# Kernel tuning notes

Measured on AMD Instinct MI355X. Metric: run time of the kernel, lower is better.

The kernel has to match this reference:

```python
import jax, jax.numpy as jnp
import numpy as np

N_NODES = 50000
N_HEDGES = 100000
N_INC = 600000
F_IN = 512
HID = 128
EPS = 1e-5
ALPHA = 0.5


def layer_norm(x, g, b):
    mu = jnp.mean(x, axis=-1, keepdims=True)
    var = jnp.mean((x - mu) ** 2, axis=-1, keepdims=True)
    return (x - mu) * jax.lax.rsqrt(var + EPS) * g + b


def scatter_mean(src, idx, num_segments):
    s = jax.ops.segment_sum(src, idx, num_segments=num_segments)
    c = jax.ops.segment_sum(jnp.ones((src.shape[0], 1), src.dtype), idx, num_segments=num_segments)
    return jnp.where(c > 0, s / jnp.maximum(c, 1.0), 0.0)


def setup_inputs() -> dict:
    key = jax.random.key(0)
    ks = jax.random.split(key, 20)

    def lin(k, fi, fo):
        kw, kb = jax.random.split(k)
        w = jax.random.normal(kw, (fi, fo), jnp.float32) / np.sqrt(fi)
        b = jax.random.normal(kb, (fo,), jnp.float32) * 0.01
        return w, b

    x1 = jax.random.normal(ks[0], (N_NODES, F_IN), jnp.float32)
    x2 = jax.random.normal(ks[1], (N_NODES, F_IN), jnp.float32)
    v1 = jax.random.randint(ks[2], (N_INC,), 0, N_NODES, jnp.int32)
    e1 = jax.random.randint(ks[3], (N_INC,), 0, N_HEDGES, jnp.int32)
    v2 = jax.random.randint(ks[4], (N_INC,), 0, N_NODES, jnp.int32)
    e2 = jax.random.randint(ks[5], (N_INC,), 0, N_HEDGES, jnp.int32)

    lin_w, lin_b = lin(ks[6], F_IN, HID)
    w1_w, w1_b = lin(ks[7], HID, HID)
    w2_w, w2_b = lin(ks[8], 2 * HID, HID)
    w_w, w_b = lin(ks[9], HID, HID)
    cls_w1, cls_b1 = lin(ks[10], HID, 64)
    cls_w2, cls_b2 = lin(ks[11], 64, 1)

    return {
        "x1": x1, "v1": v1, "e1": e1, "x2": x2, "v2": v2, "e2": e2,
        "lin_w": lin_w, "lin_b": lin_b,
        "w1_ln_g": jnp.ones((HID,)), "w1_ln_b": jnp.zeros((HID,)), "w1_w": w1_w, "w1_b": w1_b,
        "w2_ln_g": jnp.ones((2 * HID,)), "w2_ln_b": jnp.zeros((2 * HID,)), "w2_w": w2_w, "w2_b": w2_b,
        "w_ln_g": jnp.ones((HID,)), "w_ln_b": jnp.zeros((HID,)), "w_w": w_w, "w_b": w_b,
        "cls_w1": cls_w1, "cls_b1": cls_b1,
        "cls_ln_g": jnp.ones((64,)), "cls_ln_b": jnp.zeros((64,)),
        "cls_w2": cls_w2, "cls_b2": cls_b2,
    }


def _conv(X, v, e, X0, p):
    # W1 (LN + Linear) on vertices, gather to incidence pairs
    Xve = (layer_norm(X, p["w1_ln_g"], p["w1_ln_b"]) @ p["w1_w"] + p["w1_b"])[v]  # [E, H]
    Xe = scatter_mean(Xve, e, N_HEDGES)                                             # [M, H]
    Xev = Xe[e]                                                                      # [E, H]
    cat = jnp.concatenate([X[v], Xev], axis=-1)                                      # [E, 2H]
    Xev = layer_norm(cat, p["w2_ln_g"], p["w2_ln_b"]) @ p["w2_w"] + p["w2_b"]      # [E, H]
    Xv = scatter_mean(Xev, v, X.shape[0])                                            # [N, H]
    X = (1.0 - ALPHA) * Xv + ALPHA * X0
    return layer_norm(X, p["w_ln_g"], p["w_ln_b"]) @ p["w_w"] + p["w_b"]


def _branch(x, v, e, p):
    x = jax.nn.relu(x @ p["lin_w"] + p["lin_b"])
    x0 = x
    for _ in range(2):  # nlayer=2, shared conv weights
        x = jax.nn.relu(_conv(x, v, e, x0, p))
    # classifier MLP: Linear -> relu -> LN -> Linear
    h = jax.nn.relu(x @ p["cls_w1"] + p["cls_b1"])
    h = layer_norm(h, p["cls_ln_g"], p["cls_ln_b"])
    return h @ p["cls_w2"] + p["cls_b2"]


def reference(x1, v1, e1, x2, v2, e2,
              lin_w, lin_b,
              w1_ln_g, w1_ln_b, w1_w, w1_b,
              w2_ln_g, w2_ln_b, w2_w, w2_b,
              w_ln_g, w_ln_b, w_w, w_b,
              cls_w1, cls_b1, cls_ln_g, cls_ln_b, cls_w2, cls_b2):
    p = dict(lin_w=lin_w, lin_b=lin_b,
             w1_ln_g=w1_ln_g, w1_ln_b=w1_ln_b, w1_w=w1_w, w1_b=w1_b,
             w2_ln_g=w2_ln_g, w2_ln_b=w2_ln_b, w2_w=w2_w, w2_b=w2_b,
             w_ln_g=w_ln_g, w_ln_b=w_ln_b, w_w=w_w, w_b=w_b,
             cls_w1=cls_w1, cls_b1=cls_b1, cls_ln_g=cls_ln_g, cls_ln_b=cls_ln_b,
             cls_w2=cls_w2, cls_b2=cls_b2)
    return (_branch(x1, v1, e1, p), _branch(x2, v2, e2, p))
```

## Files before the change

### kernel.cpp

```cpp
#include <hip/hip_runtime.h>

#define NN 50000
#define NH 100000
#define NI 600000
#define FIN 512
#define HID 128
#define LNEPS 1e-5f

static __device__ __forceinline__ void fma4(float4& a, float s, const float4& w) {
  a.x += s * w.x; a.y += s * w.y; a.z += s * w.z; a.w += s * w.w;
}
static __device__ __forceinline__ float f4c(const float4& a, int k) {
  return k == 0 ? a.x : k == 1 ? a.y : k == 2 ? a.z : a.w;
}

__global__ void k_hist(const int* __restrict__ idx, int n, int* __restrict__ deg) {
  int i = blockIdx.x * 256 + threadIdx.x;
  if (i < n) atomicAdd(&deg[idx[i]], 1);
}

__global__ __launch_bounds__(1024) void k_scan1(int* __restrict__ data, int m,
                                                int* __restrict__ bsums) {
  __shared__ int sh[1024];
  int tid = threadIdx.x;
  int i = blockIdx.x * 1024 + tid;
  int v = (i < m) ? data[i] : 0;
  sh[tid] = v;
  __syncthreads();
  for (int off = 1; off < 1024; off <<= 1) {
    int tv = (tid >= off) ? sh[tid - off] : 0;
    __syncthreads();
    sh[tid] += tv;
    __syncthreads();
  }
  if (i < m) data[i] = sh[tid] - v;
  if (tid == 1023) bsums[blockIdx.x] = sh[1023];
}

__global__ __launch_bounds__(1024) void k_scan2(int* __restrict__ bsums, int nb) {
  __shared__ int sh[1024];
  int tid = threadIdx.x;
  int v = (tid < nb) ? bsums[tid] : 0;
  sh[tid] = v;
  __syncthreads();
  for (int off = 1; off < 1024; off <<= 1) {
    int tv = (tid >= off) ? sh[tid - off] : 0;
    __syncthreads();
    sh[tid] += tv;
    __syncthreads();
  }
  if (tid < nb) bsums[tid] = sh[tid] - v;
}

__global__ void k_scan3(int* __restrict__ data, const int* __restrict__ bsums,
                        int m, int total) {
  int i = blockIdx.x * 256 + threadIdx.x;
  if (i < m) data[i] += bsums[i >> 10];
  if (i == 0) data[m] = total;
}

__global__ void k_fill(const int* __restrict__ key, const int* __restrict__ oth, int n,
                       const int* __restrict__ starts, int* __restrict__ cursor,
                       int* __restrict__ out_oth) {
  int i = blockIdx.x * 256 + threadIdx.x;
  if (i >= n) return;
  int k = key[i];
  int pos = starts[k] + atomicAdd(&cursor[k], 1);
  out_oth[pos] = oth[i];
}

__global__ void k_sort_seg(const int* __restrict__ starts, int nseg,
                           int* __restrict__ vals) {
  int seg = blockIdx.x * 256 + threadIdx.x;
  if (seg >= nseg) return;
  int s = starts[seg], e = starts[seg + 1];
  int d = e - s;
  if (d <= 1) return;
  if (d <= 48) {
    int buf[48];
    for (int i = 0; i < d; i++) buf[i] = vals[s + i];
    for (int i = 1; i < d; i++) {
      int key = buf[i], j = i - 1;
      while (j >= 0 && buf[j] > key) { buf[j + 1] = buf[j]; j--; }
      buf[j + 1] = key;
    }
    for (int i = 0; i < d; i++) vals[s + i] = buf[i];
  } else {
    for (int i = s + 1; i < e; i++) {
      int key = vals[i], j = i - 1;
      while (j >= s && vals[j] > key) { vals[j + 1] = vals[j]; j--; }
      vals[j + 1] = key;
    }
  }
}

__global__ void k_prep_w2g(const float* __restrict__ W2, const float* __restrict__ g2,
                           float* __restrict__ W2g) {
  int i = blockIdx.x * 256 + threadIdx.x;
  if (i >= 256 * 128) return;
  int k = i >> 7;
  W2g[i] = g2[k] * W2[i];
}

__global__ __launch_bounds__(128) void k_prep_sgc0(
    const float* __restrict__ W2, const float* __restrict__ g2,
    const float* __restrict__ b2, const float* __restrict__ bias2,
    float* __restrict__ s_g, float* __restrict__ c0) {
  int t = threadIdx.x;
  float sg = 0.f, cc = 0.f;
  for (int k = 0; k < 256; k++) {
    float w = W2[k * 128 + t];
    sg += g2[k] * w;
    cc += b2[k] * w;
  }
  s_g[t] = sg;
  c0[t] = cc + bias2[t];
}

static __device__ __forceinline__ void stage_w16(float (*Wsh)[132], const float* __restrict__ W,
                                                 int row0, int t) {
  for (int s = t; s < 512; s += 256) {
    int k = s >> 5, c4 = (s & 31) * 4;
    *(float4*)&Wsh[k][c4] = *(const float4*)(W + (size_t)(row0 + k) * 128 + c4);
  }
}

static __device__ __forceinline__ void gemm128(const float (*Ash)[132], float (*Wsh)[132],
                                               const float* __restrict__ W,
                                               int t, int tc, int tr,
                                               float4 acc0[2], float4 acc1[2]) {
  for (int kk = 0; kk < 8; kk++) {
    __syncthreads();
    stage_w16(Wsh, W, kk * 16, t);
    __syncthreads();
    const int kb = kk * 16;
#pragma unroll
    for (int k4 = 0; k4 < 16; k4 += 4) {
      float4 a0 = *(const float4*)&Ash[tr * 2 + 0][kb + k4];
      float4 a1 = *(const float4*)&Ash[tr * 2 + 1][kb + k4];
#pragma unroll
      for (int kk2 = 0; kk2 < 4; kk2++) {
        float4 w0 = *(const float4*)&Wsh[k4 + kk2][tc * 4];
        float4 w1 = *(const float4*)&Wsh[k4 + kk2][64 + tc * 4];
        float a0v = f4c(a0, kk2), a1v = f4c(a1, kk2);
        fma4(acc0[0], a0v, w0); fma4(acc0[1], a0v, w1);
        fma4(acc1[0], a1v, w0); fma4(acc1[1], a1v, w1);
      }
    }
  }
}

static __device__ __forceinline__ void stage_w(float (*Wsh)[68], const float* __restrict__ W,
                                               int ldw, int row0, int col0, int t) {
  for (int s = t; s < 512; s += 256) {
    int k = s >> 4, c4 = (s & 15) * 4;
    *(float4*)&Wsh[k][c4] = *(const float4*)(W + (size_t)(row0 + k) * ldw + col0 + c4);
  }
}

static __device__ __forceinline__ void inner32(const float (*Ash)[132], const float (*Wsh)[68],
                                               int kb, int tc, int tr,
                                               float4& acc0, float4& acc1) {
#pragma unroll
  for (int k = 0; k < 32; k += 4) {
    float4 w0 = *(const float4*)&Wsh[k + 0][tc * 4];
    float4 w1 = *(const float4*)&Wsh[k + 1][tc * 4];
    float4 w2 = *(const float4*)&Wsh[k + 2][tc * 4];
    float4 w3 = *(const float4*)&Wsh[k + 3][tc * 4];
    float4 a0 = *(const float4*)&Ash[tr * 2 + 0][kb + k];
    float4 a1 = *(const float4*)&Ash[tr * 2 + 1][kb + k];
    fma4(acc0, a0.x, w0); fma4(acc0, a0.y, w1); fma4(acc0, a0.z, w2); fma4(acc0, a0.w, w3);
    fma4(acc1, a1.x, w0); fma4(acc1, a1.y, w1); fma4(acc1, a1.z, w2); fma4(acc1, a1.w, w3);
  }
}

static __device__ __forceinline__ void load_a128(float (*Ash)[132], const float* __restrict__ A,
                                                 int r0, int N, int t) {
  for (int s = t; s < 1024; s += 256) {
    int r = s >> 5, c4 = (s & 31) * 4;
    float4 val = {0, 0, 0, 0};
    if (r0 + r < N) val = *(const float4*)(A + (size_t)(r0 + r) * 128 + c4);
    *(float4*)&Ash[r][c4] = val;
  }
}

template <bool STATS>
static __device__ __forceinline__ void ln_tile(float (*Ash)[132], const float* __restrict__ g,
                                               const float* __restrict__ b,
                                               float* __restrict__ sn, float* __restrict__ qn,
                                               int r0, int N, int t) {
  int wv = t >> 6, lane = t & 63;
  for (int j = 0; j < 8; j++) {
    int r = wv * 8 + j;
    if (r0 + r < N) {
      float2 x = *(float2*)&Ash[r][lane * 2];
      float s = x.x + x.y, sq = x.x * x.x + x.y * x.y;
      for (int m = 1; m < 64; m <<= 1) { s += __shfl_xor(s, m); sq += __shfl_xor(sq, m); }
      if (STATS && lane == 0) { sn[r0 + r] = s; qn[r0 + r] = sq; }
      float mu = s * (1.f / 128.f);
      float var = sq * (1.f / 128.f) - mu * mu;
      float rstd = rsqrtf(var + LNEPS);
      float2 gg = ((const float2*)g)[lane];
      float2 bb = ((const float2*)b)[lane];
      float2 o;
      o.x = (x.x - mu) * rstd * gg.x + bb.x;
      o.y = (x.y - mu) * rstd * gg.y + bb.y;
      *(float2*)&Ash[r][lane * 2] = o;
    }
  }
}

__global__ __launch_bounds__(256) void k_proj_fused(
    const float* __restrict__ x_in, const float* __restrict__ lin_w,
    const float* __restrict__ lin_b, const float* __restrict__ w1g,
    const float* __restrict__ w1bn, const float* __restrict__ w1w,
    const float* __restrict__ w1b, float* __restrict__ X0,
    float* __restrict__ B, float* __restrict__ sn, float* __restrict__ qn, int N) {
  __shared__ float Ash[32][132];
  __shared__ float Wsh[32][68];
  float (*W16)[132] = (float(*)[132])Wsh;
  const int t = threadIdx.x;
  const int r0 = blockIdx.x * 32;
  const int tc = t & 15, tr = t >> 4;
  float4 acc0[2] = {{0,0,0,0},{0,0,0,0}}, acc1[2] = {{0,0,0,0},{0,0,0,0}};
  for (int kq = 0; kq < 4; kq++) {
    __syncthreads();
    for (int s = t; s < 1024; s += 256) {
      int r = s >> 5, c4 = (s & 31) * 4;
      float4 val = {0, 0, 0, 0};
      if (r0 + r < N) val = *(const float4*)(x_in + (size_t)(r0 + r) * 512 + kq * 128 + c4);
      *(float4*)&Ash[r][c4] = val;
    }
    gemm128((const float(*)[132])Ash, W16, lin_w + (size_t)kq * 128 * 128, t, tc, tr,
            acc0, acc1);
  }
  __syncthreads();
  for (int h = 0; h < 2; h++) {
    int c = h * 64 + tc * 4;
    float4 bb = *(const float4*)(lin_b + c);
    int row0 = r0 + tr * 2;
    float4 z0, z1;
    z0.x = fmaxf(acc0[h].x + bb.x, 0.f); z0.y = fmaxf(acc0[h].y + bb.y, 0.f);
    z0.z = fmaxf(acc0[h].z + bb.z, 0.f); z0.w = fmaxf(acc0[h].w + bb.w, 0.f);
    z1.x = fmaxf(acc1[h].x + bb.x, 0.f); z1.y = fmaxf(acc1[h].y + bb.y, 0.f);
    z1.z = fmaxf(acc1[h].z + bb.z, 0.f); z1.w = fmaxf(acc1[h].w + bb.w, 0.f);
    if (row0 < N) {
      *(float4*)(X0 + (size_t)row0 * 128 + c) = z0;
      *(float4*)&Ash[tr * 2][c] = z0;
    }
    if (row0 + 1 < N) {
      *(float4*)(X0 + (size_t)(row0 + 1) * 128 + c) = z1;
      *(float4*)&Ash[tr * 2 + 1][c] = z1;
    }
  }
  __syncthreads();
  ln_tile<true>(Ash, w1g, w1bn, sn, qn, r0, N, t);
  float4 f0[2] = {{0,0,0,0},{0,0,0,0}}, f1[2] = {{0,0,0,0},{0,0,0,0}};
  gemm128((const float(*)[132])Ash, W16, w1w, t, tc, tr, f0, f1);
  for (int h = 0; h < 2; h++) {
    int c = h * 64 + tc * 4;
    float4 bb = *(const float4*)(w1b + c);
    int row0 = r0 + tr * 2;
    if (row0 < N) {
      float4 o = {f0[h].x + bb.x, f0[h].y + bb.y, f0[h].z + bb.z, f0[h].w + bb.w};
      *(float4*)(B + (size_t)row0 * 128 + c) = o;
    }
    if (row0 + 1 < N) {
      float4 o = {f1[h].x + bb.x, f1[h].y + bb.y, f1[h].z + bb.z, f1[h].w + bb.w};
      *(float4*)(B + (size_t)(row0 + 1) * 128 + c) = o;
    }
  }
}

__global__ __launch_bounds__(256) void k_xe(
    const float* __restrict__ B, const int* __restrict__ starts,
    const int* __restrict__ vlist, float* __restrict__ Xe,
    float* __restrict__ se, float* __restrict__ qe, int M) {
  int half = threadIdx.x >> 5, lane = threadIdx.x & 31;
  int m = blockIdx.x * 8 + half;
  if (m >= M) return;
  int s = starts[m], e = starts[m + 1];
  float4 acc = {0.f, 0.f, 0.f, 0.f};
  for (int j = s; j < e; j++) {
    int vv = vlist[j];
    float4 val = ((const float4*)(B + (size_t)vv * 128))[lane];
    acc.x += val.x; acc.y += val.y; acc.z += val.z; acc.w += val.w;
  }
  int d = e - s;
  float inv = d > 0 ? 1.f / (float)d : 0.f;
  float4 o = {acc.x * inv, acc.y * inv, acc.z * inv, acc.w * inv};
  ((float4*)(Xe + (size_t)m * 128))[lane] = o;
  float ss = o.x + o.y + o.z + o.w;
  float qq = o.x * o.x + o.y * o.y + o.z * o.z + o.w * o.w;
  for (int mm = 1; mm < 32; mm <<= 1) {
    ss += __shfl_xor(ss, mm, 32);
    qq += __shfl_xor(qq, mm, 32);
  }
  if (lane == 0) { se[m] = ss; qe[m] = qq; }
}

__global__ __launch_bounds__(256) void k_nodeg(
    const float* __restrict__ X, const float* __restrict__ Xe,
    const int* __restrict__ starts_v, const int* __restrict__ e_by_v,
    const float* __restrict__ sn, const float* __restrict__ qn,
    const float* __restrict__ se, const float* __restrict__ qe,
    float* __restrict__ P, float* __restrict__ Qb,
    float* __restrict__ invdeg, float* __restrict__ t2arr, int N) {
  int half = threadIdx.x >> 5, lane = threadIdx.x & 31;
  int v = blockIdx.x * 8 + half;
  if (v >= N) return;
  int s = starts_v[v], e = starts_v[v + 1];
  float svn = sn[v], qvn = qn[v];
  float4 acc = {0.f, 0.f, 0.f, 0.f};
  float suma = 0.f, sumb = 0.f;
  for (int j = s; j < e; j++) {
    int ee = e_by_v[j];
    float mu = (svn + se[ee]) * (1.f / 256.f);
    float e2 = (qvn + qe[ee]) * (1.f / 256.f);
    float rstd = rsqrtf(e2 - mu * mu + LNEPS);
    suma += rstd;
    sumb += mu * rstd;
    float4 vv = ((const float4*)(Xe + (size_t)ee * 128))[lane];
    acc.x += rstd * vv.x; acc.y += rstd * vv.y;
    acc.z += rstd * vv.z; acc.w += rstd * vv.w;
  }
  float4 xr = ((const float4*)(X + (size_t)v * 128))[lane];
  float4 pp = {suma * xr.x, suma * xr.y, suma * xr.z, suma * xr.w};
  ((float4*)(P + (size_t)v * 128))[lane] = pp;
  ((float4*)(Qb + (size_t)v * 128))[lane] = acc;
  if (lane == 0) {
    int d = e - s;
    float inv = d > 0 ? 1.f / (float)d : 0.f;
    invdeg[v] = inv;
    t2arr[v] = sumb * inv;
  }
}

static __device__ __forceinline__ void conv2_body(
    float (*Ash)[132], float (*Wsh)[132],
    const float* __restrict__ P, const float* __restrict__ Q,
    const float* __restrict__ W, const float* __restrict__ invdeg,
    const float* __restrict__ t2arr, const float* __restrict__ s_g,
    const float* __restrict__ c0, const float* __restrict__ X0,
    const float* __restrict__ wg, const float* __restrict__ wbn,
    int r0, int N, int t, int tc, int tr) {
  float4 acc0[2] = {{0,0,0,0},{0,0,0,0}}, acc1[2] = {{0,0,0,0},{0,0,0,0}};
  for (int ph = 0; ph < 2; ph++) {
    __syncthreads();
    load_a128(Ash, ph ? Q : P, r0, N, t);
    gemm128((const float(*)[132])Ash, Wsh, W + (size_t)ph * 128 * 128, t, tc, tr,
            acc0, acc1);
  }
  __syncthreads();
  for (int r = 0; r < 2; r++) {
    int row = r0 + tr * 2 + r;
    if (row < N) {
      float t1 = invdeg[row], t2 = t2arr[row];
      float flag = t1 > 0.f ? 1.f : 0.f;
      for (int h = 0; h < 2; h++) {
        int c = h * 64 + tc * 4;
        float4 g = r ? acc1[h] : acc0[h];
        float4 sg = *(const float4*)(s_g + c);
        float4 cc = *(const float4*)(c0 + c);
        float4 x0 = *(const float4*)(X0 + (size_t)row * 128 + c);
        float4 z;
        z.x = 0.5f * (g.x * t1 - t2 * sg.x + flag * cc.x) + 0.5f * x0.x;
        z.y = 0.5f * (g.y * t1 - t2 * sg.y + flag * cc.y) + 0.5f * x0.y;
        z.z = 0.5f * (g.z * t1 - t2 * sg.z + flag * cc.z) + 0.5f * x0.z;
        z.w = 0.5f * (g.w * t1 - t2 * sg.w + flag * cc.w) + 0.5f * x0.w;
        *(float4*)&Ash[tr * 2 + r][c] = z;
      }
    }
  }
  __syncthreads();
  ln_tile<false>(Ash, wg, wbn, nullptr, nullptr, r0, N, t);
}

__global__ __launch_bounds__(256) void k_conv2w(
    const float* __restrict__ P, const float* __restrict__ Q,
    const float* __restrict__ W, const float* __restrict__ invdeg,
    const float* __restrict__ t2arr, const float* __restrict__ s_g,
    const float* __restrict__ c0, const float* __restrict__ X0,
    const float* __restrict__ wg, const float* __restrict__ wbn,
    const float* __restrict__ Ww, const float* __restrict__ wb,
    const float* __restrict__ w1g, const float* __restrict__ w1bn,
    const float* __restrict__ w1w, const float* __restrict__ w1b,
    float* __restrict__ Xout, float* __restrict__ B,
    float* __restrict__ sn, float* __restrict__ qn, int N) {
  __shared__ float Ash[32][132];
  __shared__ float Wsh[32][68];
  float (*W16)[132] = (float(*)[132])Wsh;
  const int t = threadIdx.x;
  const int r0 = blockIdx.x * 32;
  const int tc = t & 15, tr = t >> 4;
  conv2_body(Ash, W16, P, Q, W, invdeg, t2arr, s_g, c0, X0, wg, wbn, r0, N, t, tc, tr);
  float4 b0[2] = {{0,0,0,0},{0,0,0,0}}, b1[2] = {{0,0,0,0},{0,0,0,0}};
  gemm128((const float(*)[132])Ash, W16, Ww, t, tc, tr, b0, b1);
  __syncthreads();
  for (int h = 0; h < 2; h++) {
    int c = h * 64 + tc * 4;
    float4 bb = *(const float4*)(wb + c);
    int row0 = r0 + tr * 2;
    float4 z0, z1;
    z0.x = fmaxf(b0[h].x + bb.x, 0.f); z0.y = fmaxf(b0[h].y + bb.y, 0.f);
    z0.z = fmaxf(b0[h].z + bb.z, 0.f); z0.w = fmaxf(b0[h].w + bb.w, 0.f);
    z1.x = fmaxf(b1[h].x + bb.x, 0.f); z1.y = fmaxf(b1[h].y + bb.y, 0.f);
    z1.z = fmaxf(b1[h].z + bb.z, 0.f); z1.w = fmaxf(b1[h].w + bb.w, 0.f);
    if (row0 < N) {
      *(float4*)(Xout + (size_t)row0 * 128 + c) = z0;
      *(float4*)&Ash[tr * 2][c] = z0;
    }
    if (row0 + 1 < N) {
      *(float4*)(Xout + (size_t)(row0 + 1) * 128 + c) = z1;
      *(float4*)&Ash[tr * 2 + 1][c] = z1;
    }
  }
  __syncthreads();
  ln_tile<true>(Ash, w1g, w1bn, sn, qn, r0, N, t);
  float4 f0[2] = {{0,0,0,0},{0,0,0,0}}, f1[2] = {{0,0,0,0},{0,0,0,0}};
  gemm128((const float(*)[132])Ash, W16, w1w, t, tc, tr, f0, f1);
  for (int h = 0; h < 2; h++) {
    int c = h * 64 + tc * 4;
    float4 bb = *(const float4*)(w1b + c);
    int row0 = r0 + tr * 2;
    if (row0 < N) {
      float4 o = {f0[h].x + bb.x, f0[h].y + bb.y, f0[h].z + bb.z, f0[h].w + bb.w};
      *(float4*)(B + (size_t)row0 * 128 + c) = o;
    }
    if (row0 + 1 < N) {
      float4 o = {f1[h].x + bb.x, f1[h].y + bb.y, f1[h].z + bb.z, f1[h].w + bb.w};
      *(float4*)(B + (size_t)(row0 + 1) * 128 + c) = o;
    }
  }
}

__global__ __launch_bounds__(256) void k_conv2c(
    const float* __restrict__ P, const float* __restrict__ Q,
    const float* __restrict__ W, const float* __restrict__ invdeg,
    const float* __restrict__ t2arr, const float* __restrict__ s_g,
    const float* __restrict__ c0, const float* __restrict__ X0,
    const float* __restrict__ wg, const float* __restrict__ wbn,
    const float* __restrict__ Ww, const float* __restrict__ wb,
    const float* __restrict__ cw1, const float* __restrict__ cb1,
    const float* __restrict__ cg, const float* __restrict__ cbn,
    const float* __restrict__ cw2, const float* __restrict__ cb2,
    float* __restrict__ out, int N) {
  __shared__ float Ash[32][132];
  __shared__ float Wsh[32][68];
  float (*W16)[132] = (float(*)[132])Wsh;
  const int t = threadIdx.x;
  const int r0 = blockIdx.x * 32;
  const int tc = t & 15, tr = t >> 4;
  conv2_body(Ash, W16, P, Q, W, invdeg, t2arr, s_g, c0, X0, wg, wbn, r0, N, t, tc, tr);
  float4 b0[2] = {{0,0,0,0},{0,0,0,0}}, b1[2] = {{0,0,0,0},{0,0,0,0}};
  gemm128((const float(*)[132])Ash, W16, Ww, t, tc, tr, b0, b1);
  __syncthreads();
  for (int h = 0; h < 2; h++) {
    int c = h * 64 + tc * 4;
    float4 bb = *(const float4*)(wb + c);
    int row0 = r0 + tr * 2;
    if (row0 < N) {
      float4 z;
      z.x = fmaxf(b0[h].x + bb.x, 0.f); z.y = fmaxf(b0[h].y + bb.y, 0.f);
      z.z = fmaxf(b0[h].z + bb.z, 0.f); z.w = fmaxf(b0[h].w + bb.w, 0.f);
      *(float4*)&Ash[tr * 2][c] = z;
    }
    if (row0 + 1 < N) {
      float4 z;
      z.x = fmaxf(b1[h].x + bb.x, 0.f); z.y = fmaxf(b1[h].y + bb.y, 0.f);
      z.z = fmaxf(b1[h].z + bb.z, 0.f); z.w = fmaxf(b1[h].w + bb.w, 0.f);
      *(float4*)&Ash[tr * 2 + 1][c] = z;
    }
  }
  float4 h0 = {0,0,0,0}, h1 = {0,0,0,0};
  for (int kc = 0; kc < 4; kc++) {
    __syncthreads();
    stage_w(Wsh, cw1, 64, kc * 32, 0, t);
    __syncthreads();
    inner32((const float(*)[132])Ash, (const float(*)[68])Wsh, kc * 32, tc, tr, h0, h1);
  }
  __syncthreads();
  {
    int c = tc * 4;
    float4 bb = *(const float4*)(cb1 + c);
    float4 z;
    z.x = fmaxf(h0.x + bb.x, 0.f); z.y = fmaxf(h0.y + bb.y, 0.f);
    z.z = fmaxf(h0.z + bb.z, 0.f); z.w = fmaxf(h0.w + bb.w, 0.f);
    *(float4*)&Wsh[tr * 2][c] = z;
    z.x = fmaxf(h1.x + bb.x, 0.f); z.y = fmaxf(h1.y + bb.y, 0.f);
    z.z = fmaxf(h1.z + bb.z, 0.f); z.w = fmaxf(h1.w + bb.w, 0.f);
    *(float4*)&Wsh[tr * 2 + 1][c] = z;
  }
  __syncthreads();
  int wv = t >> 6, lane = t & 63;
  for (int j = 0; j < 8; j++) {
    int r = wv * 8 + j;
    if (r0 + r < N) {
      float h = Wsh[r][lane];
      float s = h, sq = h * h;
      for (int m = 1; m < 64; m <<= 1) { s += __shfl_xor(s, m); sq += __shfl_xor(sq, m); }
      float mu = s * (1.f / 64.f);
      float var = sq * (1.f / 64.f) - mu * mu;
      float rstd = rsqrtf(var + LNEPS);
      float hn = (h - mu) * rstd * cg[lane] + cbn[lane];
      float c = hn * cw2[lane];
      for (int m = 1; m < 64; m <<= 1) c += __shfl_xor(c, m);
      if (lane == 0) out[r0 + r] = c + cb2[0];
    }
  }
}

static void run_branch(const float* x_in, const int* v, const int* e,
                       const float* lin_w, const float* lin_b,
                       const float* w1g, const float* w1bn, const float* w1w, const float* w1b,
                       const float* W2g, const float* s_g, const float* c0,
                       const float* wg, const float* wbn, const float* ww, const float* wb,
                       const float* cw1, const float* cb1, const float* cg, const float* cbn,
                       const float* cw2, const float* cb2,
                       float* X, float* X0, float* B, float* Qb, float* Xe,
                       float* sn, float* qn, float* se, float* qe,
                       float* invdeg, float* t2arr,
                       int* starts_e, int* starts_v, int* cursor, int* bsums,
                       int* v_by_e, int* e_by_v,
                       float* out, hipStream_t stream) {
  const int GN = (NN + 31) / 32;
  hipMemsetAsync(starts_e, 0, (NH + 1) * sizeof(int), stream);
  k_hist<<<(NI + 255) / 256, 256, 0, stream>>>(e, NI, starts_e);
  k_scan1<<<(NH + 1023) / 1024, 1024, 0, stream>>>(starts_e, NH, bsums);
  k_scan2<<<1, 1024, 0, stream>>>(bsums, (NH + 1023) / 1024);
  k_scan3<<<(NH + 255) / 256, 256, 0, stream>>>(starts_e, bsums, NH, NI);
  hipMemsetAsync(cursor, 0, NH * sizeof(int), stream);
  k_fill<<<(NI + 255) / 256, 256, 0, stream>>>(e, v, NI, starts_e, cursor, v_by_e);
  k_sort_seg<<<(NH + 255) / 256, 256, 0, stream>>>(starts_e, NH, v_by_e);
  hipMemsetAsync(starts_v, 0, (NN + 1) * sizeof(int), stream);
  k_hist<<<(NI + 255) / 256, 256, 0, stream>>>(v, NI, starts_v);
  k_scan1<<<(NN + 1023) / 1024, 1024, 0, stream>>>(starts_v, NN, bsums);
  k_scan2<<<1, 1024, 0, stream>>>(bsums, (NN + 1023) / 1024);
  k_scan3<<<(NN + 255) / 256, 256, 0, stream>>>(starts_v, bsums, NN, NI);
  hipMemsetAsync(cursor, 0, NN * sizeof(int), stream);
  k_fill<<<(NI + 255) / 256, 256, 0, stream>>>(v, e, NI, starts_v, cursor, e_by_v);
  k_sort_seg<<<(NN + 255) / 256, 256, 0, stream>>>(starts_v, NN, e_by_v);
  k_proj_fused<<<GN, 256, 0, stream>>>(x_in, lin_w, lin_b, w1g, w1bn, w1w, w1b,
                                       X0, B, sn, qn, NN);
  for (int layer = 0; layer < 2; ++layer) {
    k_xe<<<NH / 8, 256, 0, stream>>>(B, starts_e, v_by_e, Xe, se, qe, NH);
    k_nodeg<<<(NN + 7) / 8, 256, 0, stream>>>(layer == 0 ? X0 : X, Xe, starts_v,
                                              e_by_v, sn, qn, se, qe, B, Qb,
                                              invdeg, t2arr, NN);
    if (layer == 0) {
      k_conv2w<<<GN, 256, 0, stream>>>(B, Qb, W2g, invdeg, t2arr, s_g, c0, X0,
                                       wg, wbn, ww, wb, w1g, w1bn, w1w, w1b,
                                       X, B, sn, qn, NN);
    } else {
      k_conv2c<<<GN, 256, 0, stream>>>(B, Qb, W2g, invdeg, t2arr, s_g, c0, X0,
                                       wg, wbn, ww, wb, cw1, cb1, cg, cbn,
                                       cw2, cb2, out, NN);
    }
  }
}

extern "C" void kernel_launch(void* const* d_in, const int* in_sizes, int n_in,
                              void* d_out, int out_size, void* d_ws, size_t ws_size,
                              hipStream_t stream) {
  (void)in_sizes; (void)n_in; (void)out_size; (void)ws_size;
  const float* x1 = (const float*)d_in[0];
  const int* v1 = (const int*)d_in[1];
  const int* e1 = (const int*)d_in[2];
  const float* x2 = (const float*)d_in[3];
  const int* v2 = (const int*)d_in[4];
  const int* e2 = (const int*)d_in[5];
  const float* lin_w = (const float*)d_in[6];
  const float* lin_b = (const float*)d_in[7];
  const float* w1g = (const float*)d_in[8];
  const float* w1bn = (const float*)d_in[9];
  const float* w1w = (const float*)d_in[10];
  const float* w1b = (const float*)d_in[11];
  const float* w2g = (const float*)d_in[12];
  const float* w2bn = (const float*)d_in[13];
  const float* w2w = (const float*)d_in[14];
  const float* w2b = (const float*)d_in[15];
  const float* wg = (const float*)d_in[16];
  const float* wbn = (const float*)d_in[17];
  const float* ww = (const float*)d_in[18];
  const float* wb = (const float*)d_in[19];
  const float* cw1 = (const float*)d_in[20];
  const float* cb1 = (const float*)d_in[21];
  const float* cg = (const float*)d_in[22];
  const float* cbn = (const float*)d_in[23];
  const float* cw2 = (const float*)d_in[24];
  const float* cb2 = (const float*)d_in[25];

  char* p = (char*)d_ws;
  auto alloc = [&](size_t bytes) {
    char* r = p;
    p += (bytes + 255) & ~(size_t)255;
    return r;
  };
  float* X = (float*)alloc((size_t)NN * 128 * 4);
  float* X0 = (float*)alloc((size_t)NN * 128 * 4);
  float* B = (float*)alloc((size_t)NN * 128 * 4);
  float* Qb = (float*)alloc((size_t)NN * 128 * 4);
  float* Xe = (float*)alloc((size_t)NH * 128 * 4);
  float* sn = (float*)alloc((size_t)NN * 4);
  float* qn = (float*)alloc((size_t)NN * 4);
  float* se = (float*)alloc((size_t)NH * 4);
  float* qe = (float*)alloc((size_t)NH * 4);
  float* invdeg = (float*)alloc((size_t)NN * 4);
  float* t2arr = (float*)alloc((size_t)NN * 4);
  int* starts_e = (int*)alloc((NH + 1) * 4);
  int* starts_v = (int*)alloc((NN + 1) * 4);
  int* cursor = (int*)alloc(NH * 4);
  int* bsums = (int*)alloc(1024 * 4);
  int* v_by_e = (int*)alloc((size_t)NI * 4);
  int* e_by_v = (int*)alloc((size_t)NI * 4);
  float* W2g = (float*)alloc((size_t)256 * 128 * 4);
  float* s_g = (float*)alloc(128 * 4);
  float* c0 = (float*)alloc(128 * 4);

  k_prep_w2g<<<128, 256, 0, stream>>>(w2w, w2g, W2g);
  k_prep_sgc0<<<1, 128, 0, stream>>>(w2w, w2g, w2bn, w2b, s_g, c0);

  float* out = (float*)d_out;
  run_branch(x1, v1, e1, lin_w, lin_b, w1g, w1bn, w1w, w1b, W2g, s_g, c0,
             wg, wbn, ww, wb, cw1, cb1, cg, cbn, cw2, cb2,
             X, X0, B, Qb, Xe, sn, qn, se, qe, invdeg, t2arr,
             starts_e, starts_v, cursor, bsums, v_by_e, e_by_v, out, stream);
  run_branch(x2, v2, e2, lin_w, lin_b, w1g, w1bn, w1w, w1b, W2g, s_g, c0,
             wg, wbn, ww, wb, cw1, cb1, cg, cbn, cw2, cb2,
             X, X0, B, Qb, Xe, sn, qn, se, qe, invdeg, t2arr,
             starts_e, starts_v, cursor, bsums, v_by_e, e_by_v, out + NN, stream);
}
```

Measured before the change: 1.784 ms.

## Batch CSR construction for both branches and drop P buffer write in nodeg

Builds the incidence CSR structures (histogram, scan, fill, segment sort) for both branches in shared launches, each with a doubled grid, instead of running them sequentially per branch. This halves the number of small preprocessing launches and gives each one more parallel work. Separately, k_nodeg no longer writes the P = suma*X matrix; it stores a per-node suma scalar, and the conv kernel scales X while loading the tile. That removes one full N×128 write and reread, at the cost of a few extra workspace buffers for the second branch's CSR.

```diff
diff --git a/kernel.cpp b/kernel.cpp
--- a/kernel.cpp
+++ b/kernel.cpp
@@ -14,16 +14,27 @@
   return k == 0 ? a.x : k == 1 ? a.y : k == 2 ? a.z : a.w;
 }
 
-__global__ void k_hist(const int* __restrict__ idx, int n, int* __restrict__ deg) {
-  int i = blockIdx.x * 256 + threadIdx.x;
+__global__ void k_hist2(const int* __restrict__ i1, const int* __restrict__ i2, int n,
+                        int* __restrict__ d1, int* __restrict__ d2) {
+  int nb = gridDim.x >> 1, blk = blockIdx.x;
+  bool a = blk < nb;
+  const int* idx = a ? i1 : i2;
+  int* deg = a ? d1 : d2;
+  int i = (a ? blk : blk - nb) * 256 + threadIdx.x;
   if (i < n) atomicAdd(&deg[idx[i]], 1);
 }
 
-__global__ __launch_bounds__(1024) void k_scan1(int* __restrict__ data, int m,
-                                                int* __restrict__ bsums) {
+__global__ __launch_bounds__(1024) void k_scan1_2(int* __restrict__ dd1, int* __restrict__ dd2,
+                                                  int m, int* __restrict__ b1,
+                                                  int* __restrict__ b2) {
   __shared__ int sh[1024];
+  int nb = gridDim.x >> 1, blk = blockIdx.x;
+  bool a = blk < nb;
+  int* data = a ? dd1 : dd2;
+  int* bsums = a ? b1 : b2;
+  int lb = a ? blk : blk - nb;
   int tid = threadIdx.x;
-  int i = blockIdx.x * 1024 + tid;
+  int i = lb * 1024 + tid;
   int v = (i < m) ? data[i] : 0;
   sh[tid] = v;
   __syncthreads();
@@ -34,11 +45,13 @@
     __syncthreads();
   }
   if (i < m) data[i] = sh[tid] - v;
-  if (tid == 1023) bsums[blockIdx.x] = sh[1023];
-}
-
-__global__ __launch_bounds__(1024) void k_scan2(int* __restrict__ bsums, int nb) {
+  if (tid == 1023) bsums[lb] = sh[1023];
+}
+
+__global__ __launch_bounds__(1024) void k_scan2_2(int* __restrict__ b1, int* __restrict__ b2,
+                                                  int nb) {
   __shared__ int sh[1024];
+  int* bsums = blockIdx.x == 0 ? b1 : b2;
   int tid = threadIdx.x;
   int v = (tid < nb) ? bsums[tid] : 0;
   sh[tid] = v;
@@ -52,26 +65,44 @@
   if (tid < nb) bsums[tid] = sh[tid] - v;
 }
 
-__global__ void k_scan3(int* __restrict__ data, const int* __restrict__ bsums,
-                        int m, int total) {
-  int i = blockIdx.x * 256 + threadIdx.x;
-  if (i < m) data[i] += bsums[i >> 10];
+__global__ void k_scan3_2(int* __restrict__ dd1, int* __restrict__ dd2,
+                          const int* __restrict__ b1, const int* __restrict__ b2,
+                          int m, int total) {
+  int nb = gridDim.x >> 1, blk = blockIdx.x;
+  bool a = blk < nb;
+  int* data = a ? dd1 : dd2;
+  const int* bs = a ? b1 : b2;
+  int i = (a ? blk : blk - nb) * 256 + threadIdx.x;
+  if (i < m) data[i] += bs[i >> 10];
   if (i == 0) data[m] = total;
 }
 
-__global__ void k_fill(const int* __restrict__ key, const int* __restrict__ oth, int n,
-                       const int* __restrict__ starts, int* __restrict__ cursor,
-                       int* __restrict__ out_oth) {
-  int i = blockIdx.x * 256 + threadIdx.x;
+__global__ void k_fill2(const int* __restrict__ k1, const int* __restrict__ o1,
+                        const int* __restrict__ k2, const int* __restrict__ o2, int n,
+                        const int* __restrict__ s1, const int* __restrict__ s2,
+                        int* __restrict__ c1, int* __restrict__ c2,
+                        int* __restrict__ out1, int* __restrict__ out2) {
+  int nb = gridDim.x >> 1, blk = blockIdx.x;
+  bool a = blk < nb;
+  const int* key = a ? k1 : k2;
+  const int* oth = a ? o1 : o2;
+  const int* st = a ? s1 : s2;
+  int* cur = a ? c1 : c2;
+  int* out = a ? out1 : out2;
+  int i = (a ? blk : blk - nb) * 256 + threadIdx.x;
   if (i >= n) return;
   int k = key[i];
-  int pos = starts[k] + atomicAdd(&cursor[k], 1);
-  out_oth[pos] = oth[i];
-}
-
-__global__ void k_sort_seg(const int* __restrict__ starts, int nseg,
-                           int* __restrict__ vals) {
-  int seg = blockIdx.x * 256 + threadIdx.x;
+  int pos = st[k] + atomicAdd(&cur[k], 1);
+  out[pos] = oth[i];
+}
+
+__global__ void k_sort2(const int* __restrict__ s1, const int* __restrict__ s2, int nseg,
+                        int* __restrict__ v1, int* __restrict__ v2) {
+  int nb = gridDim.x >> 1, blk = blockIdx.x;
+  bool a = blk < nb;
+  const int* starts = a ? s1 : s2;
+  int* vals = a ? v1 : v2;
+  int seg = (a ? blk : blk - nb) * 256 + threadIdx.x;
   if (seg >= nseg) return;
   int s = starts[seg], e = starts[seg + 1];
   int d = e - s;
@@ -180,6 +211,21 @@
     int r = s >> 5, c4 = (s & 31) * 4;
     float4 val = {0, 0, 0, 0};
     if (r0 + r < N) val = *(const float4*)(A + (size_t)(r0 + r) * 128 + c4);
+    *(float4*)&Ash[r][c4] = val;
+  }
+}
+
+static __device__ __forceinline__ void load_a128s(float (*Ash)[132], const float* __restrict__ A,
+                                                  const float* __restrict__ scale,
+                                                  int r0, int N, int t) {
+  for (int s = t; s < 1024; s += 256) {
+    int r = s >> 5, c4 = (s & 31) * 4;
+    float4 val = {0, 0, 0, 0};
+    if (r0 + r < N) {
+      float sc = scale[r0 + r];
+      float4 x = *(const float4*)(A + (size_t)(r0 + r) * 128 + c4);
+      val.x = sc * x.x; val.y = sc * x.y; val.z = sc * x.z; val.w = sc * x.w;
+    }
     *(float4*)&Ash[r][c4] = val;
   }
 }
@@ -300,12 +346,12 @@
 }
 
 __global__ __launch_bounds__(256) void k_nodeg(
-    const float* __restrict__ X, const float* __restrict__ Xe,
-    const int* __restrict__ starts_v, const int* __restrict__ e_by_v,
-    const float* __restrict__ sn, const float* __restrict__ qn,
-    const float* __restrict__ se, const float* __restrict__ qe,
-    float* __restrict__ P, float* __restrict__ Qb,
-    float* __restrict__ invdeg, float* __restrict__ t2arr, int N) {
+    const float* __restrict__ Xe, const int* __restrict__ starts_v,
+    const int* __restrict__ e_by_v, const float* __restrict__ sn,
+    const float* __restrict__ qn, const float* __restrict__ se,
+    const float* __restrict__ qe, float* __restrict__ Qb,
+    float* __restrict__ suma_arr, float* __restrict__ invdeg,
+    float* __restrict__ t2arr, int N) {
   int half = threadIdx.x >> 5, lane = threadIdx.x & 31;
   int v = blockIdx.x * 8 + half;
   if (v >= N) return;
@@ -324,13 +370,11 @@
     acc.x += rstd * vv.x; acc.y += rstd * vv.y;
     acc.z += rstd * vv.z; acc.w += rstd * vv.w;
   }
-  float4 xr = ((const float4*)(X + (size_t)v * 128))[lane];
-  float4 pp = {suma * xr.x, suma * xr.y, suma * xr.z, suma * xr.w};
-  ((float4*)(P + (size_t)v * 128))[lane] = pp;
   ((float4*)(Qb + (size_t)v * 128))[lane] = acc;
   if (lane == 0) {
     int d = e - s;
     float inv = d > 0 ? 1.f / (float)d : 0.f;
+    suma_arr[v] = suma;
     invdeg[v] = inv;
     t2arr[v] = sumb * inv;
   }
@@ -338,16 +382,17 @@
 
 static __device__ __forceinline__ void conv2_body(
     float (*Ash)[132], float (*Wsh)[132],
-    const float* __restrict__ P, const float* __restrict__ Q,
-    const float* __restrict__ W, const float* __restrict__ invdeg,
-    const float* __restrict__ t2arr, const float* __restrict__ s_g,
-    const float* __restrict__ c0, const float* __restrict__ X0,
-    const float* __restrict__ wg, const float* __restrict__ wbn,
-    int r0, int N, int t, int tc, int tr) {
+    const float* __restrict__ Xsrc, const float* __restrict__ suma,
+    const float* __restrict__ Q, const float* __restrict__ W,
+    const float* __restrict__ invdeg, const float* __restrict__ t2arr,
+    const float* __restrict__ s_g, const float* __restrict__ c0,
+    const float* __restrict__ X0, const float* __restrict__ wg,
+    const float* __restrict__ wbn, int r0, int N, int t, int tc, int tr) {
   float4 acc0[2] = {{0,0,0,0},{0,0,0,0}}, acc1[2] = {{0,0,0,0},{0,0,0,0}};
   for (int ph = 0; ph < 2; ph++) {
     __syncthreads();
-    load_a128(Ash, ph ? Q : P, r0, N, t);
+    if (ph == 0) load_a128s(Ash, Xsrc, suma, r0, N, t);
+    else load_a128(Ash, Q, r0, N, t);
     gemm128((const float(*)[132])Ash, Wsh, W + (size_t)ph * 128 * 128, t, tc, tr,
             acc0, acc1);
   }
@@ -377,23 +422,24 @@
 }
 
 __global__ __launch_bounds__(256) void k_conv2w(
-    const float* __restrict__ P, const float* __restrict__ Q,
-    const float* __restrict__ W, const float* __restrict__ invdeg,
-    const float* __restrict__ t2arr, const float* __restrict__ s_g,
-    const float* __restrict__ c0, const float* __restrict__ X0,
-    const float* __restrict__ wg, const float* __restrict__ wbn,
-    const float* __restrict__ Ww, const float* __restrict__ wb,
-    const float* __restrict__ w1g, const float* __restrict__ w1bn,
-    const float* __restrict__ w1w, const float* __restrict__ w1b,
-    float* __restrict__ Xout, float* __restrict__ B,
-    float* __restrict__ sn, float* __restrict__ qn, int N) {
+    const float* __restrict__ Xsrc, const float* __restrict__ suma,
+    const float* __restrict__ Q, const float* __restrict__ W,
+    const float* __restrict__ invdeg, const float* __restrict__ t2arr,
+    const float* __restrict__ s_g, const float* __restrict__ c0,
+    const float* __restrict__ X0, const float* __restrict__ wg,
+    const float* __restrict__ wbn, const float* __restrict__ Ww,
+    const float* __restrict__ wb, const float* __restrict__ w1g,
+    const float* __restrict__ w1bn, const float* __restrict__ w1w,
+    const float* __restrict__ w1b, float* __restrict__ Xout,
+    float* __restrict__ B, float* __restrict__ sn, float* __restrict__ qn, int N) {
   __shared__ float Ash[32][132];
   __shared__ float Wsh[32][68];
   float (*W16)[132] = (float(*)[132])Wsh;
   const int t = threadIdx.x;
   const int r0 = blockIdx.x * 32;
   const int tc = t & 15, tr = t >> 4;
-  conv2_body(Ash, W16, P, Q, W, invdeg, t2arr, s_g, c0, X0, wg, wbn, r0, N, t, tc, tr);
+  conv2_body(Ash, W16, Xsrc, suma, Q, W, invdeg, t2arr, s_g, c0, X0, wg, wbn,
+             r0, N, t, tc, tr);
   float4 b0[2] = {{0,0,0,0},{0,0,0,0}}, b1[2] = {{0,0,0,0},{0,0,0,0}};
   gemm128((const float(*)[132])Ash, W16, Ww, t, tc, tr, b0, b1);
   __syncthreads();
@@ -435,23 +481,24 @@
 }
 
 __global__ __launch_bounds__(256) void k_conv2c(
-    const float* __restrict__ P, const float* __restrict__ Q,
-    const float* __restrict__ W, const float* __restrict__ invdeg,
-    const float* __restrict__ t2arr, const float* __restrict__ s_g,
-    const float* __restrict__ c0, const float* __restrict__ X0,
-    const float* __restrict__ wg, const float* __restrict__ wbn,
-    const float* __restrict__ Ww, const float* __restrict__ wb,
-    const float* __restrict__ cw1, const float* __restrict__ cb1,
-    const float* __restrict__ cg, const float* __restrict__ cbn,
-    const float* __restrict__ cw2, const float* __restrict__ cb2,
-    float* __restrict__ out, int N) {
+    const float* __restrict__ Xsrc, const float* __restrict__ suma,
+    const float* __restrict__ Q, const float* __restrict__ W,
+    const float* __restrict__ invdeg, const float* __restrict__ t2arr,
+    const float* __restrict__ s_g, const float* __restrict__ c0,
+    const float* __restrict__ X0, const float* __restrict__ wg,
+    const float* __restrict__ wbn, const float* __restrict__ Ww,
+    const float* __restrict__ wb, const float* __restrict__ cw1,
+    const float* __restrict__ cb1, const float* __restrict__ cg,
+    const float* __restrict__ cbn, const float* __restrict__ cw2,
+    const float* __restrict__ cb2, float* __restrict__ out, int N) {
   __shared__ float Ash[32][132];
   __shared__ float Wsh[32][68];
   float (*W16)[132] = (float(*)[132])Wsh;
   const int t = threadIdx.x;
   const int r0 = blockIdx.x * 32;
   const int tc = t & 15, tr = t >> 4;
-  conv2_body(Ash, W16, P, Q, W, invdeg, t2arr, s_g, c0, X0, wg, wbn, r0, N, t, tc, tr);
+  conv2_body(Ash, W16, Xsrc, suma, Q, W, invdeg, t2arr, s_g, c0, X0, wg, wbn,
+             r0, N, t, tc, tr);
   float4 b0[2] = {{0,0,0,0},{0,0,0,0}}, b1[2] = {{0,0,0,0},{0,0,0,0}};
   gemm128((const float(*)[132])Ash, W16, Ww, t, tc, tr, b0, b1);
   __syncthreads();
@@ -510,7 +557,7 @@
   }
 }
 
-static void run_branch(const float* x_in, const int* v, const int* e,
+static void run_branch(const float* x_in,
                        const float* lin_w, const float* lin_b,
                        const float* w1g, const float* w1bn, const float* w1w, const float* w1b,
                        const float* W2g, const float* s_g, const float* c0,
@@ -519,41 +566,25 @@
                        const float* cw2, const float* cb2,
                        float* X, float* X0, float* B, float* Qb, float* Xe,
                        float* sn, float* qn, float* se, float* qe,
-                       float* invdeg, float* t2arr,
-                       int* starts_e, int* starts_v, int* cursor, int* bsums,
-                       int* v_by_e, int* e_by_v,
+                       float* suma, float* invdeg, float* t2arr,
+                       const int* starts_e, const int* starts_v,
+                       const int* v_by_e, const int* e_by_v,
                        float* out, hipStream_t stream) {
   const int GN = (NN + 31) / 32;
-  hipMemsetAsync(starts_e, 0, (NH + 1) * sizeof(int), stream);
-  k_hist<<<(NI + 255) / 256, 256, 0, stream>>>(e, NI, starts_e);
-  k_scan1<<<(NH + 1023) / 1024, 1024, 0, stream>>>(starts_e, NH, bsums);
-  k_scan2<<<1, 1024, 0, stream>>>(bsums, (NH + 1023) / 1024);
-  k_scan3<<<(NH + 255) / 256, 256, 0, stream>>>(starts_e, bsums, NH, NI);
-  hipMemsetAsync(cursor, 0, NH * sizeof(int), stream);
-  k_fill<<<(NI + 255) / 256, 256, 0, stream>>>(e, v, NI, starts_e, cursor, v_by_e);
-  k_sort_seg<<<(NH + 255) / 256, 256, 0, stream>>>(starts_e, NH, v_by_e);
-  hipMemsetAsync(starts_v, 0, (NN + 1) * sizeof(int), stream);
-  k_hist<<<(NI + 255) / 256, 256, 0, stream>>>(v, NI, starts_v);
-  k_scan1<<<(NN + 1023) / 1024, 1024, 0, stream>>>(starts_v, NN, bsums);
-  k_scan2<<<1, 1024, 0, stream>>>(bsums, (NN + 1023) / 1024);
-  k_scan3<<<(NN + 255) / 256, 256, 0, stream>>>(starts_v, bsums, NN, NI);
-  hipMemsetAsync(cursor, 0, NN * sizeof(int), stream);
-  k_fill<<<(NI + 255) / 256, 256, 0, stream>>>(v, e, NI, starts_v, cursor, e_by_v);
-  k_sort_seg<<<(NN + 255) / 256, 256, 0, stream>>>(starts_v, NN, e_by_v);
   k_proj_fused<<<GN, 256, 0, stream>>>(x_in, lin_w, lin_b, w1g, w1bn, w1w, w1b,
                                        X0, B, sn, qn, NN);
   for (int layer = 0; layer < 2; ++layer) {
+    const float* Xsrc = layer == 0 ? X0 : X;
     k_xe<<<NH / 8, 256, 0, stream>>>(B, starts_e, v_by_e, Xe, se, qe, NH);
-    k_nodeg<<<(NN + 7) / 8, 256, 0, stream>>>(layer == 0 ? X0 : X, Xe, starts_v,
-                                              e_by_v, sn, qn, se, qe, B, Qb,
-                                              invdeg, t2arr, NN);
+    k_nodeg<<<(NN + 7) / 8, 256, 0, stream>>>(Xe, starts_v, e_by_v, sn, qn, se, qe,
+                                              Qb, suma, invdeg, t2arr, NN);
     if (layer == 0) {
-      k_conv2w<<<GN, 256, 0, stream>>>(B, Qb, W2g, invdeg, t2arr, s_g, c0, X0,
-                                       wg, wbn, ww, wb, w1g, w1bn, w1w, w1b,
+      k_conv2w<<<GN, 256, 0, stream>>>(Xsrc, suma, Qb, W2g, invdeg, t2arr, s_g, c0,
+                                       X0, wg, wbn, ww, wb, w1g, w1bn, w1w, w1b,
                                        X, B, sn, qn, NN);
     } else {
-      k_conv2c<<<GN, 256, 0, stream>>>(B, Qb, W2g, invdeg, t2arr, s_g, c0, X0,
-                                       wg, wbn, ww, wb, cw1, cb1, cg, cbn,
+      k_conv2c<<<GN, 256, 0, stream>>>(Xsrc, suma, Qb, W2g, invdeg, t2arr, s_g, c0,
+                                       X0, wg, wbn, ww, wb, cw1, cb1, cg, cbn,
                                        cw2, cb2, out, NN);
     }
   }
@@ -605,28 +636,65 @@
   float* qn = (float*)alloc((size_t)NN * 4);
   float* se = (float*)alloc((size_t)NH * 4);
   float* qe = (float*)alloc((size_t)NH * 4);
+  float* suma = (float*)alloc((size_t)NN * 4);
   float* invdeg = (float*)alloc((size_t)NN * 4);
   float* t2arr = (float*)alloc((size_t)NN * 4);
-  int* starts_e = (int*)alloc((NH + 1) * 4);
-  int* starts_v = (int*)alloc((NN + 1) * 4);
-  int* cursor = (int*)alloc(NH * 4);
-  int* bsums = (int*)alloc(1024 * 4);
-  int* v_by_e = (int*)alloc((size_t)NI * 4);
-  int* e_by_v = (int*)alloc((size_t)NI * 4);
+  int* starts_e_all = (int*)alloc((size_t)2 * (NH + 1) * 4);
+  int* starts_v_all = (int*)alloc((size_t)2 * (NN + 1) * 4);
+  int* cursor_all = (int*)alloc((size_t)2 * NH * 4);
+  int* bsums_all = (int*)alloc((size_t)2 * 1024 * 4);
+  int* v_by_e1 = (int*)alloc((size_t)NI * 4);
+  int* v_by_e2 = (int*)alloc((size_t)NI * 4);
+  int* e_by_v1 = (int*)alloc((size_t)NI * 4);
+  int* e_by_v2 = (int*)alloc((size_t)NI * 4);
   float* W2g = (float*)alloc((size_t)256 * 128 * 4);
   float* s_g = (float*)alloc(128 * 4);
   float* c0 = (float*)alloc(128 * 4);
 
+  int* se1 = starts_e_all;
+  int* se2 = starts_e_all + (NH + 1);
+  int* sv1 = starts_v_all;
+  int* sv2 = starts_v_all + (NN + 1);
+  int* cur1 = cursor_all;
+  int* cur2 = cursor_all + NH;
+  int* bs1 = bsums_all;
+  int* bs2 = bsums_all + 1024;
+
   k_prep_w2g<<<128, 256, 0, stream>>>(w2w, w2g, W2g);
   k_prep_sgc0<<<1, 128, 0, stream>>>(w2w, w2g, w2bn, w2b, s_g, c0);
 
+  const int GBI = (NI + 255) / 256;
+  const int GBE = (NH + 1023) / 1024;
+  const int GBV = (NN + 1023) / 1024;
+  const int GHE = (NH + 255) / 256;
+  const int GHV = (NN + 255) / 256;
+
+  hipMemsetAsync(starts_e_all, 0, (size_t)2 * (NH + 1) * 4, stream);
+  k_hist2<<<2 * GBI, 256, 0, stream>>>(e1, e2, NI, se1, se2);
+  k_scan1_2<<<2 * GBE, 1024, 0, stream>>>(se1, se2, NH, bs1, bs2);
+  k_scan2_2<<<2, 1024, 0, stream>>>(bs1, bs2, GBE);
+  k_scan3_2<<<2 * GHE, 256, 0, stream>>>(se1, se2, bs1, bs2, NH, NI);
+  hipMemsetAsync(cursor_all, 0, (size_t)2 * NH * 4, stream);
+  k_fill2<<<2 * GBI, 256, 0, stream>>>(e1, v1, e2, v2, NI, se1, se2, cur1, cur2,
+                                       v_by_e1, v_by_e2);
+  k_sort2<<<2 * GHE, 256, 0, stream>>>(se1, se2, NH, v_by_e1, v_by_e2);
+  hipMemsetAsync(starts_v_all, 0, (size_t)2 * (NN + 1) * 4, stream);
+  k_hist2<<<2 * GBI, 256, 0, stream>>>(v1, v2, NI, sv1, sv2);
+  k_scan1_2<<<2 * GBV, 1024, 0, stream>>>(sv1, sv2, NN, bs1, bs2);
+  k_scan2_2<<<2, 1024, 0, stream>>>(bs1, bs2, GBV);
+  k_scan3_2<<<2 * GHV, 256, 0, stream>>>(sv1, sv2, bs1, bs2, NN, NI);
+  hipMemsetAsync(cursor_all, 0, (size_t)2 * NH * 4, stream);
+  k_fill2<<<2 * GBI, 256, 0, stream>>>(v1, e1, v2, e2, NI, sv1, sv2, cur1, cur2,
+                                       e_by_v1, e_by_v2);
+  k_sort2<<<2 * GHV, 256, 0, stream>>>(sv1, sv2, NN, e_by_v1, e_by_v2);
+
   float* out = (float*)d_out;
-  run_branch(x1, v1, e1, lin_w, lin_b, w1g, w1bn, w1w, w1b, W2g, s_g, c0,
+  run_branch(x1, lin_w, lin_b, w1g, w1bn, w1w, w1b, W2g, s_g, c0,
              wg, wbn, ww, wb, cw1, cb1, cg, cbn, cw2, cb2,
-             X, X0, B, Qb, Xe, sn, qn, se, qe, invdeg, t2arr,
-             starts_e, starts_v, cursor, bsums, v_by_e, e_by_v, out, stream);
-  run_branch(x2, v2, e2, lin_w, lin_b, w1g, w1bn, w1w, w1b, W2g, s_g, c0,
+             X, X0, B, Qb, Xe, sn, qn, se, qe, suma, invdeg, t2arr,
+             se1, sv1, v_by_e1, e_by_v1, out, stream);
+  run_branch(x2, lin_w, lin_b, w1g, w1bn, w1w, w1b, W2g, s_g, c0,
              wg, wbn, ww, wb, cw1, cb1, cg, cbn, cw2, cb2,
-             X, X0, B, Qb, Xe, sn, qn, se, qe, invdeg, t2arr,
-             starts_e, starts_v, cursor, bsums, v_by_e, e_by_v, out + NN, stream);
-}
+             X, X0, B, Qb, Xe, sn, qn, se, qe, suma, invdeg, t2arr,
+             se2, sv2, v_by_e2, e_by_v2, out + NN, stream);
+}
```

Result: faster. 1.646 ms (median of 2 runs) (-7.7%).
